# Performance work log

Measured on AMD Instinct MI355X. Metric: run time of the kernel, lower is better.

## Reference

```python
import jax, jax.numpy as jnp
import numpy as np

N = 1024  # batch


def setup_inputs() -> dict:
    key = jax.random.key(0)
    ks = jax.random.split(key, 10)
    meta_feature = jax.random.uniform(ks[0], (N, 6), dtype=jnp.float32)
    tile_wall_feature = jax.random.uniform(ks[1], (N, 34, 5), dtype=jnp.float32)
    tile_prep = jax.random.uniform(ks[2], (N, 320, 34, 7), dtype=jnp.float32)
    # keep tile_hidden_ct (channel 4) away from 0 so the division stays well-conditioned
    tile_prep = tile_prep.at[..., 4].add(0.5)
    fan_prep = jax.random.uniform(ks[3], (N, 320, 80), dtype=jnp.float32)
    redundant_tile_prep = jax.random.uniform(ks[4], (N, 320, 34), dtype=jnp.float32)
    count_prep = jax.random.uniform(ks[5], (N, 320), dtype=jnp.float32)
    chi_peng_count_remain = jax.random.uniform(ks[6], (N, 320), dtype=jnp.float32)
    # learned params: Linear(11,1) of TileProbModuleNew, fan_coeff, tile_coeff
    W_throw = jax.random.normal(ks[7], (11,), dtype=jnp.float32) * 0.05
    b_throw = jnp.array(0.5, dtype=jnp.float32)  # keeps prob_throw > 0 (faithful math; avoids NaN from neg**frac)
    fan_coeff = 0.1 + 0.015 * jax.random.normal(ks[8], (80,), dtype=jnp.float32)
    tile_coeff = 1.0 + 0.015 * jax.random.normal(ks[9], (34,), dtype=jnp.float32)
    fan_coeff_multiplier = jnp.ones((80,), dtype=jnp.float32).at[33].set(21.0)
    return {
        'meta_feature': meta_feature,
        'tile_wall_feature': tile_wall_feature,
        'tile_prep': tile_prep,
        'fan_prep': fan_prep,
        'redundant_tile_prep': redundant_tile_prep,
        'count_prep': count_prep,
        'chi_peng_count_remain': chi_peng_count_remain,
        'W_throw': W_throw,
        'b_throw': b_throw,
        'fan_coeff': fan_coeff,
        'fan_coeff_multiplier': fan_coeff_multiplier,
        'tile_coeff': tile_coeff,
    }


def reference(meta_feature, tile_wall_feature, tile_prep, fan_prep,
              redundant_tile_prep, count_prep, chi_peng_count_remain,
              W_throw, b_throw, fan_coeff, fan_coeff_multiplier, tile_coeff):
    n = meta_feature.shape[0]
    # TileProbModuleNew: per-tile Linear(11,1)
    meta_exp = jnp.broadcast_to(meta_feature[:, None, :], (n, 34, 6))
    feat = jnp.concatenate([meta_exp, tile_wall_feature], axis=-1)        # (n,34,11)
    prob_throw = feat @ W_throw + b_throw                                  # (n,34)

    tile_self_draw_baseline = tile_prep[..., 0]
    tile_need_count = tile_prep[..., 1]
    tile_cp_coeff = tile_prep[..., 2]
    tile_cp_base = tile_prep[..., 3]
    tile_hidden_ct = tile_prep[..., 4]
    tile_cp_switch = tile_prep[..., 5]
    tile_null_filler = tile_prep[..., 6]

    fan_pref = fan_prep * fan_coeff * fan_coeff_multiplier                 # (n,320,80)
    multiplied_fan_pref = jnp.sum(fan_pref, axis=-1)                       # (n,320)

    term1 = tile_self_draw_baseline * prob_throw[:, None, :] ** tile_need_count
    term2 = jnp.nan_to_num(tile_cp_base * tile_cp_coeff / tile_hidden_ct)
    terms_summed = term1 + tile_null_filler + term2 * tile_cp_switch      # (n,320,34)

    final_prob_throw = jnp.prod(terms_summed, axis=-1) * 100.0 * multiplied_fan_pref  # (n,320)

    redundant_prob = redundant_tile_prep * final_prob_throw[..., None]    # (n,320,34)
    redundant_prob = redundant_prob.reshape(n, 5, 64, 34)
    tile_bound_winrate = redundant_prob.sum(axis=2)                        # (n,5,34)

    weighted_tile_prob = (tile_bound_winrate * tile_coeff)[:, 0]           # (n,34)

    final_prob_ops = final_prob_throw.reshape(n, 5, 64).sum(axis=-1)       # (n,5)
    max_tile_prob_for_action = jnp.max(tile_bound_winrate, axis=2)         # (n,5)
    max_tile_prob_for_action = max_tile_prob_for_action.at[:, 0].set(final_prob_ops[:, 0])
    return (max_tile_prob_for_action, weighted_tile_prob)
```

## Files before the change

kernel.cpp:

```cpp
#include <hip/hip_runtime.h>
#include <math.h>

#define N_OPS 320
#define ROWS 32
#define TP_ROW 238
#define FAN_ROW 80
#define RED_ROW 34

__global__ __launch_bounds__(256) void mahjong_kernel(
    const float* __restrict__ meta,
    const float* __restrict__ wall,
    const float* __restrict__ tile_prep,
    const float* __restrict__ fan_prep,
    const float* __restrict__ redundant,
    const float* __restrict__ W_throw,
    const float* __restrict__ b_throw,
    const float* __restrict__ fan_coeff,
    const float* __restrict__ fan_mult,
    const float* __restrict__ tile_coeff,
    float* __restrict__ out_max,
    float* __restrict__ out_weighted,
    int n)
{
    const int blk  = blockIdx.x;
    const int b    = blk / 5;
    const int g    = blk % 5;
    const int tid  = threadIdx.x;
    const int wave = tid >> 6;
    const int lane = tid & 63;

    __shared__ __align__(16) float tp_sm[ROWS * TP_ROW];
    __shared__ __align__(16) float fan_sm[ROWS * FAN_ROW];
    __shared__ __align__(16) float red_sm[ROWS * RED_ROW];
    __shared__ float prob_sm[34];
    __shared__ float fc_sm[80];
    __shared__ float pprod[8][32];
    __shared__ float psum[8][32];
    __shared__ float final_sm[ROWS];
    __shared__ float acc_sm[4][34];

    if (tid < 34) {
        float acc = b_throw[0];
        #pragma unroll
        for (int j = 0; j < 6; ++j) acc += meta[(size_t)b * 6 + j] * W_throw[j];
        const float* w = wall + ((size_t)b * 34 + tid) * 5;
        #pragma unroll
        for (int j = 0; j < 5; ++j) acc += w[j] * W_throw[6 + j];
        prob_sm[tid] = acc;
    }
    if (tid >= 64 && tid < 144) {
        int f = tid - 64;
        fc_sm[f] = fan_coeff[f] * fan_mult[f];
    }

    const int s = tid >> 5;
    const int r = tid & 31;

    float acc3 = 0.0f;
    float fsum_part = 0.0f;

    for (int c = 0; c < 2; ++c) {
        const size_t row0 = (size_t)b * N_OPS + g * 64 + c * ROWS;

        __syncthreads();

        {
            const float2* src = (const float2*)(tile_prep + row0 * TP_ROW);
            float2* dst = (float2*)tp_sm;
            #pragma unroll
            for (int i = tid; i < ROWS * TP_ROW / 2; i += 256) dst[i] = src[i];
        }
        {
            const float4* src = (const float4*)(fan_prep + row0 * FAN_ROW);
            float4* dst = (float4*)fan_sm;
            #pragma unroll
            for (int i = tid; i < ROWS * FAN_ROW / 4; i += 256) dst[i] = src[i];
        }
        {
            const float2* src = (const float2*)(redundant + row0 * RED_ROW);
            float2* dst = (float2*)red_sm;
            #pragma unroll
            for (int i = tid; i < ROWS * RED_ROW / 2; i += 256) dst[i] = src[i];
        }
        __syncthreads();

        {
            const float* tpr = tp_sm + r * TP_ROW;
            float pp = 1.0f;
            #pragma unroll
            for (int t = s; t < 34; t += 8) {
                const float* e = tpr + t * 7;
                float c0 = e[0], c1 = e[1], c2 = e[2], c3 = e[3];
                float c4 = e[4], c5 = e[5], c6 = e[6];
                float term = c0 * exp2f(c1 * log2f(prob_sm[t])) + c6 + (c3 * c2 / c4) * c5;
                pp *= term;
            }
            float ps = 0.0f;
            const float* fr = fan_sm + r * FAN_ROW;
            #pragma unroll
            for (int f = s; f < 80; f += 8) ps += fr[f] * fc_sm[f];
            pprod[s][r] = pp;
            psum[s][r] = ps;
        }
        __syncthreads();

        if (tid < 32) {
            float p = 1.0f, q = 0.0f;
            #pragma unroll
            for (int s2 = 0; s2 < 8; ++s2) { p *= pprod[s2][tid]; q += psum[s2][tid]; }
            float fin = p * 100.0f * q;
            final_sm[tid] = fin;
            fsum_part += fin;
        }
        __syncthreads();

        if (lane < 34) {
            #pragma unroll
            for (int i = 0; i < 8; ++i) {
                int rr = wave * 8 + i;
                acc3 += red_sm[rr * RED_ROW + lane] * final_sm[rr];
            }
        }
    }

    if (lane < 34) acc_sm[wave][lane] = acc3;
    __syncthreads();

    if (wave == 0) {
        float tbw = 0.0f;
        if (lane < 34)
            tbw = acc_sm[0][lane] + acc_sm[1][lane] + acc_sm[2][lane] + acc_sm[3][lane];
        if (g == 0) {
            if (lane < 34)
                out_weighted[(size_t)b * 34 + lane] = tbw * tile_coeff[lane];
            float fs = fsum_part;
            #pragma unroll
            for (int sh = 1; sh < 64; sh <<= 1) fs += __shfl_xor(fs, sh);
            if (lane == 0) out_max[(size_t)b * 5] = fs;
        } else {
            float m = (lane < 34) ? tbw : -INFINITY;
            #pragma unroll
            for (int sh = 1; sh < 64; sh <<= 1) m = fmaxf(m, __shfl_xor(m, sh));
            if (lane == 0) out_max[(size_t)b * 5 + g] = m;
        }
    }
}

extern "C" void kernel_launch(void* const* d_in, const int* in_sizes, int n_in,
                              void* d_out, int out_size, void* d_ws, size_t ws_size,
                              hipStream_t stream) {
    const float* meta       = (const float*)d_in[0];
    const float* wall       = (const float*)d_in[1];
    const float* tile_prep  = (const float*)d_in[2];
    const float* fan_prep   = (const float*)d_in[3];
    const float* redundant  = (const float*)d_in[4];
    const float* W_throw    = (const float*)d_in[7];
    const float* b_throw    = (const float*)d_in[8];
    const float* fan_coeff  = (const float*)d_in[9];
    const float* fan_mult   = (const float*)d_in[10];
    const float* tile_coeff = (const float*)d_in[11];

    int n = in_sizes[0] / 6;
    float* out_max      = (float*)d_out;
    float* out_weighted = out_max + (size_t)n * 5;

    dim3 grid(n * 5), block(256);
    hipLaunchKernelGGL(mahjong_kernel, grid, block, 0, stream,
                       meta, wall, tile_prep, fan_prep, redundant,
                       W_throw, b_throw, fan_coeff, fan_mult, tile_coeff,
                       out_max, out_weighted, n);
}
```

Before: 597.4 us.

## Compute terms directly from global memory instead of staging rows in LDS

Drops the LDS staging of tile_prep, fan_prep and redundant rows. Each thread now reads its 7-channel tile element straight from global memory and stores the computed term in a small shared buffer. Fan products are reduced per float4 straight from global, and redundant values are read directly in the final accumulation. This removes the large shared buffers and one barrier per chunk and should raise occupancy. In exchange the stride-7 global reads are less coalesced, and a single 32-thread serial product over 34 terms becomes the tail step.

```diff
diff --git a/kernel.cpp b/kernel.cpp
--- a/kernel.cpp
+++ b/kernel.cpp
@@ -2,10 +2,6 @@
 #include <math.h>
 
 #define N_OPS 320
-#define ROWS 32
-#define TP_ROW 238
-#define FAN_ROW 80
-#define RED_ROW 34
 
 __global__ __launch_bounds__(256) void mahjong_kernel(
     const float* __restrict__ meta,
@@ -29,14 +25,11 @@
     const int wave = tid >> 6;
     const int lane = tid & 63;
 
-    __shared__ __align__(16) float tp_sm[ROWS * TP_ROW];
-    __shared__ __align__(16) float fan_sm[ROWS * FAN_ROW];
-    __shared__ __align__(16) float red_sm[ROWS * RED_ROW];
+    __shared__ float terms_sm[32 * 34];
+    __shared__ float qp_sm[32 * 21];
     __shared__ float prob_sm[34];
     __shared__ float fc_sm[80];
-    __shared__ float pprod[8][32];
-    __shared__ float psum[8][32];
-    __shared__ float final_sm[ROWS];
+    __shared__ float final_sm[32];
     __shared__ float acc_sm[4][34];
 
     if (tid < 34) {
@@ -52,62 +45,70 @@
         int f = tid - 64;
         fc_sm[f] = fan_coeff[f] * fan_mult[f];
     }
-
-    const int s = tid >> 5;
-    const int r = tid & 31;
+    __syncthreads();
 
     float acc3 = 0.0f;
     float fsum_part = 0.0f;
 
+    const int t_init = tid % 34;
+
     for (int c = 0; c < 2; ++c) {
-        const size_t row0 = (size_t)b * N_OPS + g * 64 + c * ROWS;
+        const size_t row0 = (size_t)b * N_OPS + g * 64 + c * 32;
 
-        __syncthreads();
+        if (c) __syncthreads();
 
         {
-            const float2* src = (const float2*)(tile_prep + row0 * TP_ROW);
-            float2* dst = (float2*)tp_sm;
+            const float* tp0 = tile_prep + row0 * 238;
+            int t = t_init;
             #pragma unroll
-            for (int i = tid; i < ROWS * TP_ROW / 2; i += 256) dst[i] = src[i];
-        }
-        {
-            const float4* src = (const float4*)(fan_prep + row0 * FAN_ROW);
-            float4* dst = (float4*)fan_sm;
-            #pragma unroll
-            for (int i = tid; i < ROWS * FAN_ROW / 4; i += 256) dst[i] = src[i];
-        }
-        {
-            const float2* src = (const float2*)(redundant + row0 * RED_ROW);
-            float2* dst = (float2*)red_sm;
-            #pragma unroll
-            for (int i = tid; i < ROWS * RED_ROW / 2; i += 256) dst[i] = src[i];
-        }
-        __syncthreads();
-
-        {
-            const float* tpr = tp_sm + r * TP_ROW;
-            float pp = 1.0f;
-            #pragma unroll
-            for (int t = s; t < 34; t += 8) {
-                const float* e = tpr + t * 7;
+            for (int k = 0; k < 4; ++k) {
+                const int tau = tid + 256 * k;
+                const float* e = tp0 + 7 * tau;
                 float c0 = e[0], c1 = e[1], c2 = e[2], c3 = e[3];
                 float c4 = e[4], c5 = e[5], c6 = e[6];
                 float term = c0 * exp2f(c1 * log2f(prob_sm[t])) + c6 + (c3 * c2 / c4) * c5;
-                pp *= term;
+                terms_sm[tau] = term;
+                t += 18; if (t >= 34) t -= 34;
             }
-            float ps = 0.0f;
-            const float* fr = fan_sm + r * FAN_ROW;
+            if (tid < 64) {
+                const int tau = 1024 + tid;
+                int t2 = tid + 4;
+                if (t2 >= 34) t2 -= 34;
+                if (t2 >= 34) t2 -= 34;
+                const float* e = tp0 + 7 * tau;
+                float c0 = e[0], c1 = e[1], c2 = e[2], c3 = e[3];
+                float c4 = e[4], c5 = e[5], c6 = e[6];
+                float term = c0 * exp2f(c1 * log2f(prob_sm[t2])) + c6 + (c3 * c2 / c4) * c5;
+                terms_sm[tau] = term;
+            }
+        }
+
+        {
+            const float4* fsrc = (const float4*)(fan_prep + row0 * 80);
             #pragma unroll
-            for (int f = s; f < 80; f += 8) ps += fr[f] * fc_sm[f];
-            pprod[s][r] = pp;
-            psum[s][r] = ps;
+            for (int k = 0; k < 3; ++k) {
+                const int i = tid + 256 * k;
+                if (i < 640) {
+                    float4 v = fsrc[i];
+                    const int r = i / 20;
+                    const int q = i - r * 20;
+                    const int f = 4 * q;
+                    qp_sm[r * 21 + q] = v.x * fc_sm[f]     + v.y * fc_sm[f + 1]
+                                      + v.z * fc_sm[f + 2] + v.w * fc_sm[f + 3];
+                }
+            }
         }
         __syncthreads();
 
         if (tid < 32) {
-            float p = 1.0f, q = 0.0f;
+            const float* tr = terms_sm + tid * 34;
+            float p = 1.0f;
             #pragma unroll
-            for (int s2 = 0; s2 < 8; ++s2) { p *= pprod[s2][tid]; q += psum[s2][tid]; }
+            for (int t = 0; t < 34; ++t) p *= tr[t];
+            const float* qr = qp_sm + tid * 21;
+            float q = 0.0f;
+            #pragma unroll
+            for (int j = 0; j < 20; ++j) q += qr[j];
             float fin = p * 100.0f * q;
             final_sm[tid] = fin;
             fsum_part += fin;
@@ -115,11 +116,10 @@
         __syncthreads();
 
         if (lane < 34) {
+            const float* rr0 = redundant + (row0 + wave * 8) * 34;
             #pragma unroll
-            for (int i = 0; i < 8; ++i) {
-                int rr = wave * 8 + i;
-                acc3 += red_sm[rr * RED_ROW + lane] * final_sm[rr];
-            }
+            for (int i = 0; i < 8; ++i)
+                acc3 += rr0[i * 34 + lane] * final_sm[wave * 8 + i];
         }
     }
 
```

Measured after the change: 512.2 us. 1.17x faster.
